# Kernel tuning notes

Measured on AMD Instinct MI355X. Metric: run time of the kernel, lower is better.

## Reference

```python
import jax, jax.numpy as jnp
import numpy as np

B, S, HID = 2, 4096, 640
NH, NKV, HD = 4, 1, 256
SCALING = 256.0 ** -0.5
SOFTCAP = 50.0
WINDOW = 512
EPS = 1e-6
ROPE_THETA = 10000.0  # local (sliding) rope base in Gemma3


def _rope_tables(seq_len, dim, theta):
    inv_freq = 1.0 / (theta ** (np.arange(0, dim, 2, dtype=np.float32) / dim))  # [dim/2]
    t = np.arange(seq_len, dtype=np.float32)
    freqs = np.outer(t, inv_freq)                      # [S, dim/2]
    emb = np.concatenate([freqs, freqs], axis=-1)      # [S, dim]
    return np.cos(emb)[None], np.sin(emb)[None]        # [1, S, dim]


def _sliding_causal_mask(b, s, window):
    i = np.arange(s)[:, None]
    j = np.arange(s)[None, :]
    allowed = (j <= i) & (j > i - window)              # causal + sliding window
    mask = np.where(allowed, 0.0, -1e9).astype(np.float32)
    return np.broadcast_to(mask[None, None], (b, 1, s, s)).copy()


def setup_inputs() -> dict:
    key = jax.random.key(0)
    ks = jax.random.split(key, 8)
    cos_np, sin_np = _rope_tables(S, HD, ROPE_THETA)
    return {
        "hidden_states": jax.random.normal(ks[0], (B, S, HID), jnp.float32),
        "cos": jnp.asarray(cos_np),
        "sin": jnp.asarray(sin_np),
        "attention_mask": jnp.asarray(_sliding_causal_mask(B, S, WINDOW)),
        "Wq": jax.random.normal(ks[1], (HID, NH * HD), jnp.float32) * 0.02,
        "Wk": jax.random.normal(ks[2], (HID, NKV * HD), jnp.float32) * 0.02,
        "Wv": jax.random.normal(ks[3], (HID, NKV * HD), jnp.float32) * 0.02,
        "Wo": jax.random.normal(ks[4], (NH * HD, HID), jnp.float32) * 0.02,
        "q_norm_w": jax.random.normal(ks[5], (HD,), jnp.float32) * 0.02,
        "k_norm_w": jax.random.normal(ks[6], (HD,), jnp.float32) * 0.02,
    }


def _rms_norm(x, w):
    var = jnp.mean(jnp.square(x), axis=-1, keepdims=True)
    return x * jax.lax.rsqrt(var + EPS) * (1.0 + w)


def _rotate_half(x):
    x1, x2 = jnp.split(x, 2, axis=-1)
    return jnp.concatenate([-x2, x1], axis=-1)


def _apply_rope(x, cos, sin):
    # x: [B, H, S, D]; cos/sin: [1, S, D] -> unsqueeze head dim
    c = cos[:, None, :, :]
    s = sin[:, None, :, :]
    return x * c + _rotate_half(x) * s


def reference(hidden_states, cos, sin, attention_mask, Wq, Wk, Wv, Wo, q_norm_w, k_norm_w):
    b, s, _ = hidden_states.shape
    # projections (no bias)
    q = (hidden_states @ Wq).reshape(b, s, NH, HD).transpose(0, 2, 1, 3)   # [B,NH,S,D]
    k = (hidden_states @ Wk).reshape(b, s, NKV, HD).transpose(0, 2, 1, 3)  # [B,1,S,D]
    v = (hidden_states @ Wv).reshape(b, s, NKV, HD).transpose(0, 2, 1, 3)  # [B,1,S,D]
    # per-head RMSNorm on q/k
    q = _rms_norm(q, q_norm_w)
    k = _rms_norm(k, k_norm_w)
    # RoPE
    q = _apply_rope(q, cos, sin)
    k = _apply_rope(k, cos, sin)
    # GQA: single kv head broadcast to all query heads
    k2 = k[:, 0]  # [B,S,D]
    v2 = v[:, 0]  # [B,S,D]
    scores = jnp.einsum('bhqd,bkd->bhqk', q, k2) * SCALING
    scores = SOFTCAP * jnp.tanh(scores / SOFTCAP)          # logit softcapping
    scores = scores + attention_mask                        # causal + sliding window
    attn = jax.nn.softmax(scores, axis=-1)
    out = jnp.einsum('bhqk,bkd->bhqd', attn, v2)            # [B,NH,S,D]
    out = out.transpose(0, 2, 1, 3).reshape(b, s, NH * HD)  # [B,S,NH*D]
    return out @ Wo                                         # [B,S,HID]
```

## Files before the change

kernel.cpp:

```cpp
#include <hip/hip_runtime.h>

typedef unsigned short u16;
typedef unsigned int u32;

typedef __attribute__((ext_vector_type(8)))  short bf16x8;
typedef __attribute__((ext_vector_type(4)))  float f32x4;

__device__ __forceinline__ float b2f(u16 u) {
    union { unsigned int i; float f; } v; v.i = ((unsigned int)u) << 16; return v.f;
}
__device__ __forceinline__ u16 f2b(float f) {
    union { float ff; unsigned int i; } v; v.ff = f;
    unsigned int x = v.i;
    return (u16)((x + 0x7fffu + ((x >> 16) & 1u)) >> 16);
}
__device__ __forceinline__ bool detect_bf16(const void* cosT) {
    return ((*(const u32*)cosT) & 0xffffu) == 0x3f80u;
}
__device__ __forceinline__ float4 ld4(const void* p, size_t off, bool isbf) {
    if (isbf) {
        ushort4 v = *(const ushort4*)((const u16*)p + off);
        return make_float4(b2f(v.x), b2f(v.y), b2f(v.z), b2f(v.w));
    }
    return *(const float4*)((const float*)p + off);
}
__device__ __forceinline__ float lds1(const void* p, size_t off, bool isbf) {
    return isbf ? b2f(((const u16*)p)[off]) : ((const float*)p)[off];
}
__device__ __forceinline__ void gll16(const void* g, void* l) {
    __builtin_amdgcn_global_load_lds(
        (const __attribute__((address_space(1))) u32*)g,
        (__attribute__((address_space(3))) u32*)l, 16, 0, 0);
}
__device__ __forceinline__ float capmask(float sdot, int i, int j) {
    float v = sdot * (0.0625f / 50.0f);
    v = fminf(fmaxf(v, -10.0f), 10.0f);
    float e = __expf(2.0f * v);
    float c = 50.0f * (e - 1.0f) / (e + 1.0f);
    bool allowed = (j <= i) && (j > i - 512);
    return allowed ? c : -1e30f;
}

__global__ __launch_bounds__(256) void prep(
    const void* __restrict__ hidden,
    const void* __restrict__ Wq, const void* __restrict__ Wk,
    const void* __restrict__ Wv, const void* __restrict__ Wo,
    const void* __restrict__ cosT,
    u16* __restrict__ Hb, u16* __restrict__ WT, u16* __restrict__ WoT)
{
    const bool isbf = detect_bf16(cosT);
    __shared__ float T[32][33];
    int id = blockIdx.x;
    if (id < 2560) {
        size_t base = ((size_t)id * 256 + threadIdx.x) * 8;
        if (isbf) {
            *(uint4*)(Hb + base) = *(const uint4*)((const u16*)hidden + base);
        } else {
            float4 a = ld4(hidden, base, false);
            float4 b = ld4(hidden, base + 4, false);
            uint4 o;
            o.x = (u32)f2b(a.x) | ((u32)f2b(a.y) << 16);
            o.y = (u32)f2b(a.z) | ((u32)f2b(a.w) << 16);
            o.z = (u32)f2b(b.x) | ((u32)f2b(b.y) << 16);
            o.w = (u32)f2b(b.z) | ((u32)f2b(b.w) << 16);
            *(uint4*)(Hb + base) = o;
        }
        return;
    }
    id -= 2560;
    const int tx = threadIdx.x & 31, ty = threadIdx.x >> 5;
    if (id < 960) {
        const int n0 = (id % 48) * 32, k0 = (id / 48) * 32;
        const void* src; int ldw, nof;
        if (n0 < 1024)      { src = Wq; ldw = 1024; nof = n0; }
        else if (n0 < 1280) { src = Wk; ldw = 256;  nof = n0 - 1024; }
        else                { src = Wv; ldw = 256;  nof = n0 - 1280; }
#pragma unroll
        for (int j = 0; j < 4; j++)
            T[ty + 8 * j][tx] = lds1(src, (size_t)(k0 + ty + 8 * j) * ldw + nof + tx, isbf);
        __syncthreads();
#pragma unroll
        for (int j = 0; j < 4; j++)
            WT[(size_t)(n0 + ty + 8 * j) * 640 + k0 + tx] = f2b(T[tx][ty + 8 * j]);
    } else {
        id -= 960;
        const int k0 = (id & 31) * 32, n0 = (id >> 5) * 32;
#pragma unroll
        for (int j = 0; j < 4; j++)
            T[ty + 8 * j][tx] = lds1(Wo, (size_t)(k0 + ty + 8 * j) * 640 + n0 + tx, isbf);
        __syncthreads();
#pragma unroll
        for (int j = 0; j < 4; j++)
            WoT[(size_t)(n0 + ty + 8 * j) * 1024 + k0 + tx] = f2b(T[tx][ty + 8 * j]);
    }
}

__global__ __launch_bounds__(256) void qkv_gemm(
    const u16* __restrict__ Hb, const u16* __restrict__ WT,
    u16* __restrict__ Qb, u16* __restrict__ Kb, u16* __restrict__ Vtg)
{
    const int n0 = blockIdx.x * 128, m0 = blockIdx.y * 128;
    const int t = threadIdx.x, w = t >> 6, lane = t & 63;
    const int l15 = lane & 15, quad = lane >> 4;
    const int wm = (w & 1) * 64, wn = (w >> 1) * 64;

    __shared__ __align__(16) char smem[33792];

    f32x4 acc[4][4];
#pragma unroll
    for (int i = 0; i < 4; i++)
#pragma unroll
        for (int j = 0; j < 4; j++) acc[i][j] = (f32x4)0.0f;

#pragma unroll
    for (int i = 0; i < 2; i++) {
        int ci = t + 256 * i, m = ci >> 2, c = ci & 3;
        gll16(Hb + (size_t)(m0 + m) * 640 + c * 8, smem + ci * 16);
        gll16(WT + (size_t)(n0 + m) * 640 + c * 8, smem + 8192 + ci * 16);
    }
    __syncthreads();

    for (int it = 0; it < 20; ++it) {
        const int kb = it * 32;
        char* cur = smem + (it & 1) * 16384;
        if (it < 19) {
            char* nxt = smem + ((it + 1) & 1) * 16384;
#pragma unroll
            for (int i = 0; i < 2; i++) {
                int ci = t + 256 * i, m = ci >> 2, c = ci & 3;
                gll16(Hb + (size_t)(m0 + m) * 640 + kb + 32 + c * 8, nxt + ci * 16);
                gll16(WT + (size_t)(n0 + m) * 640 + kb + 32 + c * 8, nxt + 8192 + ci * 16);
            }
        }
        const u16 (*Ah)[32] = (const u16 (*)[32])cur;
        const u16 (*Bh)[32] = (const u16 (*)[32])(cur + 8192);
        bf16x8 af[4], bfr[4];
#pragma unroll
        for (int mi = 0; mi < 4; mi++)
            af[mi] = *(const bf16x8*)&Ah[wm + mi * 16 + l15][quad * 8];
#pragma unroll
        for (int ni = 0; ni < 4; ni++)
            bfr[ni] = *(const bf16x8*)&Bh[wn + ni * 16 + l15][quad * 8];
#pragma unroll
        for (int mi = 0; mi < 4; mi++)
#pragma unroll
            for (int ni = 0; ni < 4; ni++)
                acc[mi][ni] = __builtin_amdgcn_mfma_f32_16x16x32_bf16(
                    af[mi], bfr[ni], acc[mi][ni], 0, 0, 0);
        __syncthreads();
    }

    if (n0 >= 1280) {
        const int bb = m0 >> 12, sblk = m0 & 4095;
#pragma unroll
        for (int mi = 0; mi < 4; mi++)
#pragma unroll
            for (int ni = 0; ni < 4; ni++) {
                int vd = n0 + wn + ni * 16 + l15 - 1280;
                int sb = sblk + wm + mi * 16 + quad * 4;
                ushort4 vv = make_ushort4(f2b(acc[mi][ni][0]), f2b(acc[mi][ni][1]),
                                          f2b(acc[mi][ni][2]), f2b(acc[mi][ni][3]));
                *(ushort4*)(Vtg + (size_t)bb * 1048576 + (size_t)vd * 4096 + sb) = vv;
            }
        return;
    }

    u16 (*Sc)[132] = (u16 (*)[132])smem;
#pragma unroll
    for (int mi = 0; mi < 4; mi++)
#pragma unroll
        for (int ni = 0; ni < 4; ni++)
#pragma unroll
            for (int r = 0; r < 4; r++)
                Sc[wm + mi * 16 + quad * 4 + r][wn + ni * 16 + l15] = f2b(acc[mi][ni][r]);
    __syncthreads();

    u16* dst; int ldo, coff;
    if (n0 < 1024) { dst = Qb; ldo = 1024; coff = n0; }
    else           { dst = Kb; ldo = 256;  coff = n0 - 1024; }
#pragma unroll
    for (int i = 0; i < 8; i++) {
        int idx = t + 256 * i, r = idx >> 4, c = idx & 15;
        *(uint4*)(dst + (size_t)(m0 + r) * ldo + coff + c * 8) = *(const uint4*)&Sc[r][c * 8];
    }
}

__global__ __launch_bounds__(320) void norm_rope(
    u16* __restrict__ Qb, u16* __restrict__ Kb,
    const void* __restrict__ cosT, const void* __restrict__ sinT,
    const void* __restrict__ qw, const void* __restrict__ kw)
{
    const bool isbf = detect_bf16(cosT);
    const int row = blockIdx.x, s = row & 4095;
    const int g = threadIdx.x >> 6, lane = threadIdx.x & 63, d0 = lane * 4;

    u16* p; const void* w;
    if (g < 4) { p = Qb + (size_t)row * 1024 + g * 256 + d0; w = qw; }
    else       { p = Kb + (size_t)row * 256 + d0;            w = kw; }

    ushort4 xv = *(const ushort4*)p;
    float x0 = b2f(xv.x), x1 = b2f(xv.y), x2 = b2f(xv.z), x3 = b2f(xv.w);
    float ssum = x0 * x0 + x1 * x1 + x2 * x2 + x3 * x3;
#pragma unroll
    for (int off = 32; off > 0; off >>= 1) ssum += __shfl_xor(ssum, off, 64);
    float rs = rsqrtf(ssum * (1.0f / 256.0f) + 1e-6f);

    float4 wv = ld4(w, d0, isbf);
    float n0 = x0 * rs * (1.0f + wv.x);
    float n1 = x1 * rs * (1.0f + wv.y);
    float n2 = x2 * rs * (1.0f + wv.z);
    float n3 = x3 * rs * (1.0f + wv.w);

    float o0 = __shfl_xor(n0, 32, 64);
    float o1 = __shfl_xor(n1, 32, 64);
    float o2 = __shfl_xor(n2, 32, 64);
    float o3 = __shfl_xor(n3, 32, 64);
    float sgn = (lane < 32) ? -1.0f : 1.0f;

    float4 cv = ld4(cosT, (size_t)s * 256 + d0, isbf);
    float4 sv = ld4(sinT, (size_t)s * 256 + d0, isbf);
    *(ushort4*)p = make_ushort4(
        f2b(n0 * cv.x + sgn * o0 * sv.x), f2b(n1 * cv.y + sgn * o1 * sv.y),
        f2b(n2 * cv.z + sgn * o2 * sv.z), f2b(n3 * cv.w + sgn * o3 * sv.w));
}

__global__ __launch_bounds__(512, 2) void attn_mfma(
    const u16* __restrict__ Qb, const u16* __restrict__ Kb,
    const u16* __restrict__ Vtg, u16* __restrict__ AO)
{
    const int bx = blockIdx.x;
    const int q0 = (((bx & 7) << 4) + (bx >> 3)) * 32;
    const int b  = blockIdx.y;
    const int t = threadIdx.x, w = t >> 6, lane = t & 63;
    const int h = w & 3, qh = w >> 2;
    const int l15 = lane & 15, quad = lane >> 4;
    const int qbase = q0 + qh * 16;

    __shared__ __align__(16) u16 Ks[64][264];
    __shared__ __align__(16) u16 Vt[256][72];
    __shared__ __align__(16) u16 Pr[8][16][72];
    __shared__ float l_s[8][16];

    bf16x8 qf[8];
    {
        const u16* qp = Qb + ((size_t)(b * 4096 + qbase + l15)) * 1024 + h * 256 + quad * 8;
#pragma unroll
        for (int s = 0; s < 8; s++) qf[s] = *(const bf16x8*)(qp + s * 32);
    }

    f32x4 o[16];
#pragma unroll
    for (int i = 0; i < 16; i++) o[i] = (f32x4)0.0f;
    float lp[4] = {0.f, 0.f, 0.f, 0.f};

    const int lo = q0 - 511;
    const int jb0 = lo > 0 ? (lo >> 6) << 6 : 0;
    const int jb1 = (q0 + 31) & ~63;

    const u16* kbase = Kb + (size_t)b * 4096 * 256;
    const u16* vbase = Vtg + (size_t)b * 1048576;

    for (int jb = jb0; jb <= jb1; jb += 64) {
        __syncthreads();
#pragma unroll
        for (int i = 0; i < 4; i++) {
            int ci = t + 512 * i;
            *(uint4*)&Ks[ci >> 5][(ci & 31) * 8] =
                *(const uint4*)(kbase + (size_t)(jb + (ci >> 5)) * 256 + (ci & 31) * 8);
            *(uint4*)&Vt[ci >> 3][(ci & 7) * 8] =
                *(const uint4*)(vbase + (size_t)(ci >> 3) * 4096 + jb + (ci & 7) * 8);
        }
        __syncthreads();

        f32x4 s[4];
#pragma unroll
        for (int a = 0; a < 4; a++) s[a] = (f32x4)0.0f;
#pragma unroll
        for (int ds = 0; ds < 8; ds++) {
#pragma unroll
            for (int a = 0; a < 4; a++) {
                bf16x8 kf = *(const bf16x8*)&Ks[a * 16 + l15][ds * 32 + quad * 8];
                s[a] = __builtin_amdgcn_mfma_f32_16x16x32_bf16(qf[ds], kf, s[a], 0, 0, 0);
            }
        }
#pragma unroll
        for (int ap = 0; ap < 2; ap++) {
            const int j0 = jb + ap * 32 + l15;
#pragma unroll
            for (int r = 0; r < 4; r++) {
                int qi = qbase + quad * 4 + r;
                float p0 = __expf(capmask(s[2 * ap][r],     qi, j0));
                float p1 = __expf(capmask(s[2 * ap + 1][r], qi, j0 + 16));
                u16 pb0 = f2b(p0), pb1 = f2b(p1);
                Pr[w][quad * 4 + r][ap * 32 + l15]      = pb0;
                Pr[w][quad * 4 + r][ap * 32 + 16 + l15] = pb1;
                lp[r] += b2f(pb0) + b2f(pb1);
            }
        }
        __threadfence_block();
        bf16x8 pf0 = *(const bf16x8*)&Pr[w][l15][quad * 8];
        bf16x8 pf1 = *(const bf16x8*)&Pr[w][l15][32 + quad * 8];
#pragma unroll
        for (int mt = 0; mt < 16; mt++) {
            bf16x8 vf0 = *(const bf16x8*)&Vt[mt * 16 + l15][quad * 8];
            o[mt] = __builtin_amdgcn_mfma_f32_16x16x32_bf16(vf0, pf0, o[mt], 0, 0, 0);
        }
#pragma unroll
        for (int mt = 0; mt < 16; mt++) {
            bf16x8 vf1 = *(const bf16x8*)&Vt[mt * 16 + l15][32 + quad * 8];
            o[mt] = __builtin_amdgcn_mfma_f32_16x16x32_bf16(vf1, pf1, o[mt], 0, 0, 0);
        }
    }

#pragma unroll
    for (int r = 0; r < 4; r++) {
        float v = lp[r];
        v += __shfl_xor(v, 1, 64); v += __shfl_xor(v, 2, 64);
        v += __shfl_xor(v, 4, 64); v += __shfl_xor(v, 8, 64);
        lp[r] = v;
    }
    if (l15 == 0) {
#pragma unroll
        for (int r = 0; r < 4; r++) l_s[w][quad * 4 + r] = lp[r];
    }
    __threadfence_block();
    __syncthreads();
    const float inv = 1.0f / l_s[w][l15];

    u16* aop = AO + ((size_t)(b * 4096 + qbase + l15)) * 1024 + h * 256 + quad * 4;
#pragma unroll
    for (int mt = 0; mt < 16; mt++) {
        *(ushort4*)(aop + mt * 16) = make_ushort4(
            f2b(o[mt][0] * inv), f2b(o[mt][1] * inv),
            f2b(o[mt][2] * inv), f2b(o[mt][3] * inv));
    }
}

__global__ __launch_bounds__(256) void out_gemm(
    const u16* __restrict__ AO, const u16* __restrict__ WoT,
    const void* __restrict__ cosT, void* __restrict__ outp)
{
    const bool isbf = detect_bf16(cosT);
    const int n0 = blockIdx.x * 64, m0 = blockIdx.y * 128;
    const int t = threadIdx.x, w = t >> 6, lane = t & 63;
    const int l15 = lane & 15, quad = lane >> 4;
    const int wm = (w & 1) * 64, wn = (w >> 1) * 32;

    __shared__ __align__(16) char smem[34816];

    f32x4 acc[4][2];
#pragma unroll
    for (int i = 0; i < 4; i++)
#pragma unroll
        for (int j = 0; j < 2; j++) acc[i][j] = (f32x4)0.0f;

    {
#pragma unroll
        for (int i = 0; i < 2; i++) {
            int ci = t + 256 * i, m = ci >> 2, c = ci & 3;
            gll16(AO + (size_t)(m0 + m) * 1024 + c * 8, smem + ci * 16);
        }
        int m = t >> 2, c = t & 3;
        gll16(WoT + (size_t)(n0 + m) * 1024 + c * 8, smem + 8192 + t * 16);
    }
    __syncthreads();

    for (int it = 0; it < 32; ++it) {
        const int kb = it * 32;
        char* cur = smem + (it & 1) * 12288;
        if (it < 31) {
            char* nxt = smem + ((it + 1) & 1) * 12288;
#pragma unroll
            for (int i = 0; i < 2; i++) {
                int ci = t + 256 * i, m = ci >> 2, c = ci & 3;
                gll16(AO + (size_t)(m0 + m) * 1024 + kb + 32 + c * 8, nxt + ci * 16);
            }
            int m = t >> 2, c = t & 3;
            gll16(WoT + (size_t)(n0 + m) * 1024 + kb + 32 + c * 8, nxt + 8192 + t * 16);
        }
        const u16 (*Ah)[32] = (const u16 (*)[32])cur;
        const u16 (*Bh)[32] = (const u16 (*)[32])(cur + 8192);
        bf16x8 af[4], bfr[2];
#pragma unroll
        for (int mi = 0; mi < 4; mi++)
            af[mi] = *(const bf16x8*)&Ah[wm + mi * 16 + l15][quad * 8];
#pragma unroll
        for (int ni = 0; ni < 2; ni++)
            bfr[ni] = *(const bf16x8*)&Bh[wn + ni * 16 + l15][quad * 8];
#pragma unroll
        for (int mi = 0; mi < 4; mi++)
#pragma unroll
            for (int ni = 0; ni < 2; ni++)
                acc[mi][ni] = __builtin_amdgcn_mfma_f32_16x16x32_bf16(
                    af[mi], bfr[ni], acc[mi][ni], 0, 0, 0);
        __syncthreads();
    }

    float (*Scf)[68] = (float (*)[68])smem;
#pragma unroll
    for (int mi = 0; mi < 4; mi++)
#pragma unroll
        for (int ni = 0; ni < 2; ni++)
#pragma unroll
            for (int r = 0; r < 4; r++)
                Scf[wm + mi * 16 + quad * 4 + r][wn + ni * 16 + l15] = acc[mi][ni][r];
    __syncthreads();

    if (isbf) {
#pragma unroll
        for (int i = 0; i < 4; i++) {
            int idx = t + 256 * i, r = idx >> 3, c = idx & 7;
            ushort4 lo4 = make_ushort4(
                f2b(Scf[r][c * 8 + 0]), f2b(Scf[r][c * 8 + 1]),
                f2b(Scf[r][c * 8 + 2]), f2b(Scf[r][c * 8 + 3]));
            ushort4 hi4 = make_ushort4(
                f2b(Scf[r][c * 8 + 4]), f2b(Scf[r][c * 8 + 5]),
                f2b(Scf[r][c * 8 + 6]), f2b(Scf[r][c * 8 + 7]));
            u16* p = (u16*)outp + (size_t)(m0 + r) * 640 + n0 + c * 8;
            *(ushort4*)p = lo4; *(ushort4*)(p + 4) = hi4;
        }
    } else {
#pragma unroll
        for (int i = 0; i < 8; i++) {
            int idx = t + 256 * i, r = idx >> 4, c = idx & 15;
            float4 v = *(const float4*)&Scf[r][c * 4];
            *(float4*)((float*)outp + (size_t)(m0 + r) * 640 + n0 + c * 4) = v;
        }
    }
}

extern "C" void kernel_launch(void* const* d_in, const int* in_sizes, int n_in,
                              void* d_out, int out_size, void* d_ws, size_t ws_size,
                              hipStream_t stream) {
    const void* hidden = d_in[0];
    const void* cosT   = d_in[1];
    const void* sinT   = d_in[2];
    const void* Wq     = d_in[4];
    const void* Wk     = d_in[5];
    const void* Wv     = d_in[6];
    const void* Wo     = d_in[7];
    const void* qw     = d_in[8];
    const void* kw     = d_in[9];

    char* ws = (char*)d_ws;
    u16* Hb  = (u16*)ws;
    u16* WT  = (u16*)(ws + 10485760);
    u16* AO  = (u16*)ws;
    u16* WoT = (u16*)(ws + 16777216);
    u16* Qb  = (u16*)(ws + 18087936);
    u16* Kb  = (u16*)(ws + 34865152);
    u16* Vtg = (u16*)(ws + 39059456);

    prep<<<dim3(4160), 256, 0, stream>>>(hidden, Wq, Wk, Wv, Wo, cosT, Hb, WT, WoT);
    qkv_gemm<<<dim3(12, 64), 256, 0, stream>>>(Hb, WT, Qb, Kb, Vtg);
    norm_rope<<<dim3(8192), 320, 0, stream>>>(Qb, Kb, cosT, sinT, qw, kw);
    attn_mfma<<<dim3(128, 2), 512, 0, stream>>>(Qb, Kb, Vtg, AO);
    out_gemm<<<dim3(10, 64), 256, 0, stream>>>(AO, WoT, cosT, d_out);
}
```

Baseline: 310.9 us.

## Fuse Q norm/RoPE into attention, coalesce V stores, swizzle GEMM block order

Q RMSNorm and RoPE now run inside the attention kernel when Q fragments are loaded from registers. This removes the separate read-modify-write pass over Q, and the norm kernel now handles only K. The transposed V output in the QKV GEMM goes through shared memory so it is written as coalesced 16-byte rows instead of scattered 8-byte stores. Both GEMMs use a 1D grid with an XCD-style block swizzle to improve L2 locality. The trade-off is extra per-block arithmetic and cos/sin loads in attention, plus a little more register pressure.

```diff
diff --git a/kernel.cpp b/kernel.cpp
--- a/kernel.cpp
+++ b/kernel.cpp
@@ -99,7 +99,9 @@
     const u16* __restrict__ Hb, const u16* __restrict__ WT,
     u16* __restrict__ Qb, u16* __restrict__ Kb, u16* __restrict__ Vtg)
 {
-    const int n0 = blockIdx.x * 128, m0 = blockIdx.y * 128;
+    const int bid = blockIdx.x;
+    const int sw = (bid & 7) * 96 + (bid >> 3);
+    const int n0 = (sw % 12) * 128, m0 = (sw / 12) * 128;
     const int t = threadIdx.x, w = t >> 6, lane = t & 63;
     const int l15 = lane & 15, quad = lane >> 4;
     const int wm = (w & 1) * 64, wn = (w >> 1) * 64;
@@ -150,22 +152,26 @@
         __syncthreads();
     }
 
+    u16 (*Sc)[132] = (u16 (*)[132])smem;
     if (n0 >= 1280) {
-        const int bb = m0 >> 12, sblk = m0 & 4095;
+        const int bb = m0 >> 12, sblk = m0 & 4095, vd0 = n0 - 1280;
 #pragma unroll
         for (int mi = 0; mi < 4; mi++)
 #pragma unroll
-            for (int ni = 0; ni < 4; ni++) {
-                int vd = n0 + wn + ni * 16 + l15 - 1280;
-                int sb = sblk + wm + mi * 16 + quad * 4;
-                ushort4 vv = make_ushort4(f2b(acc[mi][ni][0]), f2b(acc[mi][ni][1]),
-                                          f2b(acc[mi][ni][2]), f2b(acc[mi][ni][3]));
-                *(ushort4*)(Vtg + (size_t)bb * 1048576 + (size_t)vd * 4096 + sb) = vv;
-            }
+            for (int ni = 0; ni < 4; ni++)
+#pragma unroll
+                for (int r = 0; r < 4; r++)
+                    Sc[wn + ni * 16 + l15][wm + mi * 16 + quad * 4 + r] = f2b(acc[mi][ni][r]);
+        __syncthreads();
+#pragma unroll
+        for (int i = 0; i < 8; i++) {
+            int idx = t + 256 * i, vd = idx >> 4, c = idx & 15;
+            *(uint4*)(Vtg + (size_t)bb * 1048576 + (size_t)(vd0 + vd) * 4096 + sblk + c * 8) =
+                *(const uint4*)&Sc[vd][c * 8];
+        }
         return;
     }
 
-    u16 (*Sc)[132] = (u16 (*)[132])smem;
 #pragma unroll
     for (int mi = 0; mi < 4; mi++)
 #pragma unroll
@@ -185,18 +191,16 @@
     }
 }
 
-__global__ __launch_bounds__(320) void norm_rope(
-    u16* __restrict__ Qb, u16* __restrict__ Kb,
+__global__ __launch_bounds__(256) void norm_rope_k(
+    u16* __restrict__ Kb,
     const void* __restrict__ cosT, const void* __restrict__ sinT,
-    const void* __restrict__ qw, const void* __restrict__ kw)
+    const void* __restrict__ kw)
 {
     const bool isbf = detect_bf16(cosT);
-    const int row = blockIdx.x, s = row & 4095;
-    const int g = threadIdx.x >> 6, lane = threadIdx.x & 63, d0 = lane * 4;
-
-    u16* p; const void* w;
-    if (g < 4) { p = Qb + (size_t)row * 1024 + g * 256 + d0; w = qw; }
-    else       { p = Kb + (size_t)row * 256 + d0;            w = kw; }
+    const int row = blockIdx.x * 4 + (threadIdx.x >> 6), s = row & 4095;
+    const int lane = threadIdx.x & 63, d0 = lane * 4;
+
+    u16* p = Kb + (size_t)row * 256 + d0;
 
     ushort4 xv = *(const ushort4*)p;
     float x0 = b2f(xv.x), x1 = b2f(xv.y), x2 = b2f(xv.z), x3 = b2f(xv.w);
@@ -205,7 +209,7 @@
     for (int off = 32; off > 0; off >>= 1) ssum += __shfl_xor(ssum, off, 64);
     float rs = rsqrtf(ssum * (1.0f / 256.0f) + 1e-6f);
 
-    float4 wv = ld4(w, d0, isbf);
+    float4 wv = ld4(kw, d0, isbf);
     float n0 = x0 * rs * (1.0f + wv.x);
     float n1 = x1 * rs * (1.0f + wv.y);
     float n2 = x2 * rs * (1.0f + wv.z);
@@ -226,7 +230,10 @@
 
 __global__ __launch_bounds__(512, 2) void attn_mfma(
     const u16* __restrict__ Qb, const u16* __restrict__ Kb,
-    const u16* __restrict__ Vtg, u16* __restrict__ AO)
+    const u16* __restrict__ Vtg,
+    const void* __restrict__ cosT, const void* __restrict__ sinT,
+    const void* __restrict__ qw,
+    u16* __restrict__ AO)
 {
     const int bx = blockIdx.x;
     const int q0 = (((bx & 7) << 4) + (bx >> 3)) * 32;
@@ -235,6 +242,7 @@
     const int h = w & 3, qh = w >> 2;
     const int l15 = lane & 15, quad = lane >> 4;
     const int qbase = q0 + qh * 16;
+    const bool isbf = detect_bf16(cosT);
 
     __shared__ __align__(16) u16 Ks[64][264];
     __shared__ __align__(16) u16 Vt[256][72];
@@ -243,9 +251,51 @@
 
     bf16x8 qf[8];
     {
-        const u16* qp = Qb + ((size_t)(b * 4096 + qbase + l15)) * 1024 + h * 256 + quad * 8;
-#pragma unroll
-        for (int s = 0; s < 8; s++) qf[s] = *(const bf16x8*)(qp + s * 32);
+        const int srow = qbase + l15;
+        const u16* qp = Qb + ((size_t)(b * 4096 + srow)) * 1024 + h * 256 + quad * 8;
+        float x[8][8];
+        float ss = 0.f;
+#pragma unroll
+        for (int s8 = 0; s8 < 8; s8++) {
+            ushort4 a = *(const ushort4*)(qp + s8 * 32);
+            ushort4 c = *(const ushort4*)(qp + s8 * 32 + 4);
+            x[s8][0] = b2f(a.x); x[s8][1] = b2f(a.y); x[s8][2] = b2f(a.z); x[s8][3] = b2f(a.w);
+            x[s8][4] = b2f(c.x); x[s8][5] = b2f(c.y); x[s8][6] = b2f(c.z); x[s8][7] = b2f(c.w);
+#pragma unroll
+            for (int j = 0; j < 8; j++) ss += x[s8][j] * x[s8][j];
+        }
+        ss += __shfl_xor(ss, 16, 64);
+        ss += __shfl_xor(ss, 32, 64);
+        const float rs = rsqrtf(ss * (1.0f / 256.0f) + 1e-6f);
+#pragma unroll
+        for (int s8 = 0; s8 < 8; s8++) {
+            const int d0 = quad * 8 + s8 * 32;
+            float4 w0 = ld4(qw, d0, isbf), w1 = ld4(qw, d0 + 4, isbf);
+            x[s8][0] *= rs * (1.0f + w0.x); x[s8][1] *= rs * (1.0f + w0.y);
+            x[s8][2] *= rs * (1.0f + w0.z); x[s8][3] *= rs * (1.0f + w0.w);
+            x[s8][4] *= rs * (1.0f + w1.x); x[s8][5] *= rs * (1.0f + w1.y);
+            x[s8][6] *= rs * (1.0f + w1.z); x[s8][7] *= rs * (1.0f + w1.w);
+        }
+#pragma unroll
+        for (int s8 = 0; s8 < 8; s8++) {
+            const int d0 = quad * 8 + s8 * 32;
+            const size_t co = (size_t)srow * 256 + d0;
+            float4 c0 = ld4(cosT, co, isbf), c1 = ld4(cosT, co + 4, isbf);
+            float4 s0 = ld4(sinT, co, isbf), s1 = ld4(sinT, co + 4, isbf);
+            const float sgn = (s8 < 4) ? -1.0f : 1.0f;
+            const int sp = s8 ^ 4;
+            u16 r0 = f2b(x[s8][0] * c0.x + sgn * x[sp][0] * s0.x);
+            u16 r1 = f2b(x[s8][1] * c0.y + sgn * x[sp][1] * s0.y);
+            u16 r2 = f2b(x[s8][2] * c0.z + sgn * x[sp][2] * s0.z);
+            u16 r3 = f2b(x[s8][3] * c0.w + sgn * x[sp][3] * s0.w);
+            u16 r4 = f2b(x[s8][4] * c1.x + sgn * x[sp][4] * s1.x);
+            u16 r5 = f2b(x[s8][5] * c1.y + sgn * x[sp][5] * s1.y);
+            u16 r6 = f2b(x[s8][6] * c1.z + sgn * x[sp][6] * s1.z);
+            u16 r7 = f2b(x[s8][7] * c1.w + sgn * x[sp][7] * s1.w);
+            short rr[8] = {(short)r0, (short)r1, (short)r2, (short)r3,
+                           (short)r4, (short)r5, (short)r6, (short)r7};
+            qf[s8] = *(const bf16x8*)rr;
+        }
     }
 
     f32x4 o[16];
@@ -341,7 +391,9 @@
     const void* __restrict__ cosT, void* __restrict__ outp)
 {
     const bool isbf = detect_bf16(cosT);
-    const int n0 = blockIdx.x * 64, m0 = blockIdx.y * 128;
+    const int bid = blockIdx.x;
+    const int sw = (bid & 7) * 80 + (bid >> 3);
+    const int n0 = (sw % 10) * 64, m0 = (sw / 10) * 128;
     const int t = threadIdx.x, w = t >> 6, lane = t & 63;
     const int l15 = lane & 15, quad = lane >> 4;
     const int wm = (w & 1) * 64, wn = (w >> 1) * 32;
@@ -452,8 +504,8 @@
     u16* Vtg = (u16*)(ws + 39059456);
 
     prep<<<dim3(4160), 256, 0, stream>>>(hidden, Wq, Wk, Wv, Wo, cosT, Hb, WT, WoT);
-    qkv_gemm<<<dim3(12, 64), 256, 0, stream>>>(Hb, WT, Qb, Kb, Vtg);
-    norm_rope<<<dim3(8192), 320, 0, stream>>>(Qb, Kb, cosT, sinT, qw, kw);
-    attn_mfma<<<dim3(128, 2), 512, 0, stream>>>(Qb, Kb, Vtg, AO);
-    out_gemm<<<dim3(10, 64), 256, 0, stream>>>(AO, WoT, cosT, d_out);
-}
+    qkv_gemm<<<dim3(768), 256, 0, stream>>>(Hb, WT, Qb, Kb, Vtg);
+    norm_rope_k<<<dim3(2048), 256, 0, stream>>>(Kb, cosT, sinT, kw);
+    attn_mfma<<<dim3(128, 2), 512, 0, stream>>>(Qb, Kb, Vtg, cosT, sinT, qw, AO);
+    out_gemm<<<dim3(640), 256, 0, stream>>>(AO, WoT, cosT, d_out);
+}
```

After: 324.5 us. +4.3%, slower.
